# Kernel tuning notes

Measured on AMD Instinct MI355X. Metric: run time of the kernel, lower is better.

## Reference

```python
import jax, jax.numpy as jnp
import numpy as np

B, S, D, H, K = 64, 512, 1024, 1024, 4
DT = 0.05
TAU_MIN, TAU_MAX = 0.01, 10.0


def setup_inputs() -> dict:
    key = jax.random.key(0)
    ks = jax.random.split(key, 5)
    x = jax.random.normal(ks[0], (B, S, D), dtype=jnp.float32)
    # complexity signal [B,1]; positive like a variance
    complexity = jax.random.uniform(ks[1], (B, 1), dtype=jnp.float32) + 0.5
    # orthogonal-ish recurrent weight (scaled normal) and xavier-ish input weight
    W_rec = jax.random.normal(ks[2], (H, H), dtype=jnp.float32) / np.float32(np.sqrt(H))
    W_in = jax.random.normal(ks[3], (D, H), dtype=jnp.float32) * np.float32(np.sqrt(2.0 / (D + H)))
    bias = jnp.zeros((H,), dtype=jnp.float32)
    tau_bands = jnp.logspace(np.log10(TAU_MIN), np.log10(TAU_MAX), K, dtype=jnp.float32)
    mixer_w = jax.random.normal(ks[4], (K, 1), dtype=jnp.float32)  # nn.Linear(1, K).weight
    mixer_b = jnp.zeros((K,), dtype=jnp.float32)                   # nn.Linear(1, K).bias
    return dict(x=x, complexity=complexity, W_rec=W_rec, W_in=W_in,
                bias=bias, tau_bands=tau_bands, mixer_w=mixer_w, mixer_b=mixer_b)


def reference(x, complexity, W_rec, W_in, bias, tau_bands, mixer_w, mixer_b):
    # tau mixing: Linear(1,K) on complexity -> softmax -> convex mix of tau bands
    tau_logits = complexity @ mixer_w.T + mixer_b          # [B, K]
    w = jax.nn.softmax(tau_logits, axis=-1)                # [B, K]
    mixed_tau = jnp.sum(tau_bands[None, :] * w, axis=1)    # [B]
    alpha = jnp.exp(-DT / mixed_tau)[:, None]              # [B, 1] -> broadcasts over H

    h0 = jnp.zeros((x.shape[0], W_rec.shape[0]), dtype=x.dtype)

    def step(h, xt):
        # h_{t+1} = a*h + (1-a)*tanh(h @ W_rec^T + x_t @ W_in^T + b)
        pre = h @ W_rec.T + xt @ W_in.T + bias
        h_new = alpha * h + (1.0 - alpha) * jnp.tanh(pre)
        return h_new, h_new

    h_final, outs = jax.lax.scan(step, h0, jnp.swapaxes(x, 0, 1))  # scan over time
    output = jnp.swapaxes(outs, 0, 1)                               # [B, S, H]
    return output, h_final
```

## Files before the change

kernel.cpp:

```cpp
#include <hip/hip_runtime.h>
#include <math.h>

#define BATCH 64
#define SEQ 512
#define DIM 1024
#define HID 1024
#define KBANDS 4
#define DT_C 0.05f
#define CNT_STRIDE 32

typedef short bf16x8 __attribute__((ext_vector_type(8)));
typedef float f32x4 __attribute__((ext_vector_type(4)));

__device__ __forceinline__ unsigned bf16rn(float x) {
    unsigned u = __float_as_uint(x);
    return (u + 0x7fffu + ((u >> 16) & 1u)) >> 16;
}

__device__ __forceinline__ void splitf(float f, unsigned short* hi, unsigned short* lo) {
    unsigned h = bf16rn(f);
    float r = f - __uint_as_float(h << 16);
    *hi = (unsigned short)h;
    *lo = (unsigned short)bf16rn(r);
}

__device__ __forceinline__ void split_bf16(float4 f, ushort4* hi, ushort4* lo) {
    unsigned short h0, h1, h2, h3, l0, l1, l2, l3;
    splitf(f.x, &h0, &l0); splitf(f.y, &h1, &l1);
    splitf(f.z, &h2, &l2); splitf(f.w, &h3, &l3);
    *hi = make_ushort4(h0, h1, h2, h3);
    *lo = make_ushort4(l0, l1, l2, l3);
}

__global__ void alpha_kernel(const float* __restrict__ complexity,
                             const float* __restrict__ tau_bands,
                             const float* __restrict__ mixer_w,
                             const float* __restrict__ mixer_b,
                             float* __restrict__ alpha) {
    int b = threadIdx.x;
    if (b < BATCH) {
        float c = complexity[b];
        float lg[KBANDS];
        float mx = -1e30f;
        #pragma unroll
        for (int k = 0; k < KBANDS; k++) {
            lg[k] = c * mixer_w[k] + mixer_b[k];
            mx = fmaxf(mx, lg[k]);
        }
        float se = 0.f, tau = 0.f;
        #pragma unroll
        for (int k = 0; k < KBANDS; k++) {
            float e = expf(lg[k] - mx);
            se += e;
            tau += tau_bands[k] * e;
        }
        tau /= se;
        alpha[b] = expf(-DT_C / tau);
    }
}

__global__ __launch_bounds__(256) void win_split(const float* __restrict__ win,
                                                 unsigned short* __restrict__ whi,
                                                 unsigned short* __restrict__ wlo) {
    size_t i = ((size_t)blockIdx.x * 256 + threadIdx.x) * 4;
    float4 f = *(const float4*)(win + i);
    ushort4 h4, l4;
    split_bf16(f, &h4, &l4);
    *(ushort4*)(whi + i) = h4;
    *(ushort4*)(wlo + i) = l4;
}

#define RP 272
#define IG_LDS (4 * 64 * RP)

__global__ __launch_bounds__(256) void in_gemm_mfma(const float* __restrict__ x,
                                                    const unsigned short* __restrict__ whi,
                                                    const unsigned short* __restrict__ wlo,
                                                    const float* __restrict__ bias,
                                                    float* __restrict__ out) {
    extern __shared__ char lg[];
    char* Ahi = lg;
    char* Alo = lg + 64 * RP;
    char* Bhi = lg + 2 * 64 * RP;
    char* Blo = lg + 3 * 64 * RP;

    int tid  = threadIdx.x;
    int m0   = blockIdx.x * 64;
    int n0   = blockIdx.y * 64;
    int lane = tid & 63;
    int w    = tid >> 6;
    int row  = lane & 15;
    int kq   = lane >> 4;

    int srow = tid >> 2;
    int skeg = (tid & 3) * 32;

    const float* xsrc = x + (size_t)(m0 + srow) * 1024 + skeg;
    const unsigned short* bhsrc = whi + (size_t)(n0 + srow) * 1024 + skeg;
    const unsigned short* blsrc = wlo + (size_t)(n0 + srow) * 1024 + skeg;
    char* dah = Ahi + srow * RP + skeg * 2;
    char* dal = Alo + srow * RP + skeg * 2;
    char* dbh = Bhi + srow * RP + skeg * 2;
    char* dbl = Blo + srow * RP + skeg * 2;

    f32x4 acc[4];
    #pragma unroll
    for (int mt = 0; mt < 4; mt++) acc[mt] = (f32x4){0.f, 0.f, 0.f, 0.f};

    for (int k0 = 0; k0 < 1024; k0 += 128) {
        #pragma unroll
        for (int i = 0; i < 8; i++) {
            float4 f = *(const float4*)(xsrc + k0 + i * 4);
            ushort4 h4, l4;
            split_bf16(f, &h4, &l4);
            *(ushort4*)(dah + i * 8) = h4;
            *(ushort4*)(dal + i * 8) = l4;
        }
        #pragma unroll
        for (int i = 0; i < 4; i++) {
            *(float4*)(dbh + i * 16) = *(const float4*)(bhsrc + k0 + i * 8);
            *(float4*)(dbl + i * 16) = *(const float4*)(blsrc + k0 + i * 8);
        }
        __syncthreads();
        #pragma unroll
        for (int ks = 0; ks < 4; ks++) {
            int koff = (ks * 32 + kq * 8) * 2;
            bf16x8 bh = *(const bf16x8*)(Bhi + (w * 16 + row) * RP + koff);
            bf16x8 bl = *(const bf16x8*)(Blo + (w * 16 + row) * RP + koff);
            #pragma unroll
            for (int mt = 0; mt < 4; mt++) {
                bf16x8 ah = *(const bf16x8*)(Ahi + (mt * 16 + row) * RP + koff);
                bf16x8 al = *(const bf16x8*)(Alo + (mt * 16 + row) * RP + koff);
                acc[mt] = __builtin_amdgcn_mfma_f32_16x16x32_bf16(ah, bh, acc[mt], 0, 0, 0);
                acc[mt] = __builtin_amdgcn_mfma_f32_16x16x32_bf16(al, bh, acc[mt], 0, 0, 0);
                acc[mt] = __builtin_amdgcn_mfma_f32_16x16x32_bf16(ah, bl, acc[mt], 0, 0, 0);
            }
        }
        __syncthreads();
    }
    int n = n0 + w * 16 + (lane & 15);
    float bn = bias[n];
    #pragma unroll
    for (int mt = 0; mt < 4; mt++)
        #pragma unroll
        for (int r = 0; r < 4; r++)
            out[(size_t)(m0 + mt * 16 + kq * 4 + r) * 1024 + n] = acc[mt][r] + bn;
}


#define HPITCH 2064
#define LDS_HI  0
#define LDS_LO  33024
#define LDS_RED 66048
#define LDS_TOTAL 70144
#define HB_PLANE 131072
#define HB_SLOT  262144

__global__ __launch_bounds__(256, 1) void recur_coop(const float* __restrict__ Wrec,
                                                     const float* __restrict__ alpha,
                                                     float* __restrict__ out,
                                                     int* __restrict__ cnt,
                                                     unsigned short* __restrict__ hbuf) {
    extern __shared__ char lbase[];

    int tid  = threadIdx.x;
    int bs   = blockIdx.x & 3;
    int js   = blockIdx.x >> 2;
    int lane = tid & 63;
    int w    = tid >> 6;
    int row  = lane & 15;
    int kq   = lane >> 4;

    bf16x8 wh[8], wl[8];
    {
        const float* wsrc = Wrec + (size_t)(js * 16 + row) * HID + w * 256 + kq * 8;
        #pragma unroll
        for (int ks = 0; ks < 8; ks++) {
            float4 f0 = *(const float4*)(wsrc + ks * 32);
            float4 f1 = *(const float4*)(wsrc + ks * 32 + 4);
            union { unsigned short u[8]; bf16x8 v; } H, L;
            splitf(f0.x, &H.u[0], &L.u[0]);
            splitf(f0.y, &H.u[1], &L.u[1]);
            splitf(f0.z, &H.u[2], &L.u[2]);
            splitf(f0.w, &H.u[3], &L.u[3]);
            splitf(f1.x, &H.u[4], &L.u[4]);
            splitf(f1.y, &H.u[5], &L.u[5]);
            splitf(f1.z, &H.u[6], &L.u[6]);
            splitf(f1.w, &H.u[7], &L.u[7]);
            wh[ks] = H.v;
            wl[ks] = L.v;
        }
    }

    int eb = tid >> 4;
    int ej = tid & 15;
    int bglob = bs * 16 + eb;
    int jglob = js * 16 + ej;
    float a_reg = alpha[bglob];
    float om = 1.f - a_reg;
    float* xwp = out + (size_t)bglob * SEQ * HID + jglob;

    int srow = tid >> 4, sl16 = tid & 15;
    const char* hb_lane = (const char*)hbuf + (size_t)(bs * 16 + srow) * 2048 + sl16 * 16;
    char* ph_base = (char*)hbuf + (size_t)bglob * 2048 + jglob * 2;

    float hp = 0.f;
    float* redp = (float*)(lbase + LDS_RED);
    const char* ah_base = lbase + LDS_HI + row * HPITCH + (w * 256 + kq * 8) * 2;
    const char* al_base = lbase + LDS_LO + row * HPITCH + (w * 256 + kq * 8) * 2;
    char* dh = lbase + LDS_HI + srow * HPITCH + sl16 * 16;
    char* dl = lbase + LDS_LO + srow * HPITCH + sl16 * 16;

    for (int t = 0; t < SEQ; t++) {
        float xw = *xwp;
        float sum = 0.f;
        if (t > 0) {
            if (tid == 0) {
                int* cp = cnt + (size_t)((t - 1) * 4 + bs) * CNT_STRIDE;
                int spins = 0;
                while (__hip_atomic_load(cp, __ATOMIC_RELAXED,
                                         __HIP_MEMORY_SCOPE_AGENT) < 64) {
                    __builtin_amdgcn_s_sleep(1);
                    if (++spins >= 8192) {
                        spins = 0;
                        if (__hip_atomic_fetch_add(cp, 0, __ATOMIC_RELAXED,
                                __HIP_MEMORY_SCOPE_AGENT) >= 64) break;
                    }
                }
            }
            __syncthreads();
            {
                const char* bh = hb_lane + (size_t)((t - 1) & 1) * HB_SLOT;
                const char* bl = bh + HB_PLANE;
                float4 v[16];
                #pragma unroll
                for (int it = 0; it < 8; it++)
                    asm volatile("global_load_dwordx4 %0, %1, off offset:%2 sc0 sc1"
                                 : "=v"(v[it]) : "v"(bh), "i"(it * 256) : "memory");
                #pragma unroll
                for (int it = 0; it < 8; it++)
                    asm volatile("global_load_dwordx4 %0, %1, off offset:%2 sc0 sc1"
                                 : "=v"(v[8 + it]) : "v"(bl), "i"(it * 256) : "memory");
                asm volatile("s_waitcnt vmcnt(0)" ::: "memory");
                #pragma unroll
                for (int it = 0; it < 8; it++)
                    *(float4*)(dh + it * 256) = v[it];
                #pragma unroll
                for (int it = 0; it < 8; it++)
                    *(float4*)(dl + it * 256) = v[8 + it];
            }
            __syncthreads();
            f32x4 acc0 = {0.f, 0.f, 0.f, 0.f};
            f32x4 acc1 = {0.f, 0.f, 0.f, 0.f};
            #pragma unroll
            for (int ks = 0; ks < 8; ks++) {
                bf16x8 ah = *(const bf16x8*)(ah_base + ks * 64);
                bf16x8 al = *(const bf16x8*)(al_base + ks * 64);
                if (ks & 1) {
                    acc1 = __builtin_amdgcn_mfma_f32_16x16x32_bf16(ah, wh[ks], acc1, 0, 0, 0);
                    acc1 = __builtin_amdgcn_mfma_f32_16x16x32_bf16(al, wh[ks], acc1, 0, 0, 0);
                    acc1 = __builtin_amdgcn_mfma_f32_16x16x32_bf16(ah, wl[ks], acc1, 0, 0, 0);
                } else {
                    acc0 = __builtin_amdgcn_mfma_f32_16x16x32_bf16(ah, wh[ks], acc0, 0, 0, 0);
                    acc0 = __builtin_amdgcn_mfma_f32_16x16x32_bf16(al, wh[ks], acc0, 0, 0, 0);
                    acc0 = __builtin_amdgcn_mfma_f32_16x16x32_bf16(ah, wl[ks], acc0, 0, 0, 0);
                }
            }
            #pragma unroll
            for (int r = 0; r < 4; r++)
                redp[w * 256 + (kq * 4 + r) * 16 + row] = acc0[r] + acc1[r];
            __syncthreads();
            sum = redp[tid] + redp[256 + tid] + redp[512 + tid] + redp[768 + tid];
        }
        float pre = sum + xw;
        float hn = a_reg * hp + om * tanhf(pre);
        *xwp = hn;
        if (t == SEQ - 1)
            out[(size_t)BATCH * SEQ * HID + (size_t)bglob * HID + jglob] = hn;
        {
            unsigned short hi16, lo16;
            splitf(hn, &hi16, &lo16);
            unsigned hv = hi16, lv = lo16;
            char* ph = ph_base + (size_t)(t & 1) * HB_SLOT;
            char* pl = ph + HB_PLANE;
            asm volatile("global_store_short %0, %1, off sc0 sc1"
                         :: "v"(ph), "v"(hv) : "memory");
            asm volatile("global_store_short %0, %1, off sc0 sc1"
                         :: "v"(pl), "v"(lv) : "memory");
        }
        asm volatile("s_waitcnt vmcnt(0)" ::: "memory");
        __syncthreads();
        if (tid == 0)
            __hip_atomic_fetch_add(cnt + (size_t)(t * 4 + bs) * CNT_STRIDE, 1,
                    __ATOMIC_RELAXED, __HIP_MEMORY_SCOPE_AGENT);
        hp = hn;
        xwp += HID;
    }
}

extern "C" void kernel_launch(void* const* d_in, const int* in_sizes, int n_in,
                              void* d_out, int out_size, void* d_ws, size_t ws_size,
                              hipStream_t stream) {
    const float* x          = (const float*)d_in[0];
    const float* complexity = (const float*)d_in[1];
    const float* Wrec       = (const float*)d_in[2];
    const float* Win        = (const float*)d_in[3];
    const float* bias       = (const float*)d_in[4];
    const float* tau_bands  = (const float*)d_in[5];
    const float* mixer_w    = (const float*)d_in[6];
    const float* mixer_b    = (const float*)d_in[7];
    float* out = (float*)d_out;

    float* alpha = (float*)d_ws;
    int*   cnt   = (int*)((char*)d_ws + 256);
    unsigned short* whi  = (unsigned short*)((char*)d_ws + 266240);
    unsigned short* wlo  = (unsigned short*)((char*)d_ws + 266240 + 2097152);
    unsigned short* hbuf = (unsigned short*)((char*)d_ws + 266240 + 4194304);

    hipMemsetAsync(cnt, 0, SEQ * 4 * CNT_STRIDE * sizeof(int), stream);
    alpha_kernel<<<1, 64, 0, stream>>>(complexity, tau_bands, mixer_w, mixer_b, alpha);
    win_split<<<1024, 256, 0, stream>>>(Win, whi, wlo);

    hipFuncSetAttribute((const void*)in_gemm_mfma,
                        hipFuncAttributeMaxDynamicSharedMemorySize, IG_LDS);
    in_gemm_mfma<<<dim3(512, 16), 256, IG_LDS, stream>>>(x, whi, wlo, bias, out);

    hipFuncSetAttribute((const void*)recur_coop,
                        hipFuncAttributeMaxDynamicSharedMemorySize, LDS_TOTAL);
    void* args[] = { (void*)&Wrec, (void*)&alpha, (void*)&out, (void*)&cnt, (void*)&hbuf };
    hipLaunchCooperativeKernel((void*)recur_coop, dim3(256), dim3(256),
                               args, LDS_TOTAL, stream);
}
```

Measured before the change: 2.544 ms.

## Retile input GEMM so each block covers full N, reading W_in from global

The input-projection GEMM now uses 512-thread blocks that each compute a 64x1024 output slab. A block splits its x tile to bf16 hi/lo pairs once and shares it in LDS across 8 waves. B fragments (W_in hi/lo) are loaded directly from global memory per wave instead of being staged in LDS. This removes the 16x redundant reading and splitting of x across the old N-grid. It risks high register pressure from 32 accumulators per lane and uncoalesced, LDS-free B loads served only by cache.

Result: faster. 2.460 ms (-3.3%).

```diff
diff --git a/kernel.cpp b/kernel.cpp
--- a/kernel.cpp
+++ b/kernel.cpp
@@ -71,9 +71,9 @@
 }
 
 #define RP 272
-#define IG_LDS (4 * 64 * RP)
-
-__global__ __launch_bounds__(256) void in_gemm_mfma(const float* __restrict__ x,
+#define IG_LDS (2 * 64 * RP)
+
+__global__ __launch_bounds__(512) void in_gemm_mfma(const float* __restrict__ x,
                                                     const unsigned short* __restrict__ whi,
                                                     const unsigned short* __restrict__ wlo,
                                                     const float* __restrict__ bias,
@@ -81,70 +81,72 @@
     extern __shared__ char lg[];
     char* Ahi = lg;
     char* Alo = lg + 64 * RP;
-    char* Bhi = lg + 2 * 64 * RP;
-    char* Blo = lg + 3 * 64 * RP;
 
     int tid  = threadIdx.x;
     int m0   = blockIdx.x * 64;
-    int n0   = blockIdx.y * 64;
     int lane = tid & 63;
     int w    = tid >> 6;
     int row  = lane & 15;
     int kq   = lane >> 4;
 
-    int srow = tid >> 2;
-    int skeg = (tid & 3) * 32;
-
+    int srow = tid >> 3;
+    int skeg = (tid & 7) * 16;
     const float* xsrc = x + (size_t)(m0 + srow) * 1024 + skeg;
-    const unsigned short* bhsrc = whi + (size_t)(n0 + srow) * 1024 + skeg;
-    const unsigned short* blsrc = wlo + (size_t)(n0 + srow) * 1024 + skeg;
     char* dah = Ahi + srow * RP + skeg * 2;
     char* dal = Alo + srow * RP + skeg * 2;
-    char* dbh = Bhi + srow * RP + skeg * 2;
-    char* dbl = Blo + srow * RP + skeg * 2;
-
-    f32x4 acc[4];
+
+    f32x4 acc[4][8];
     #pragma unroll
-    for (int mt = 0; mt < 4; mt++) acc[mt] = (f32x4){0.f, 0.f, 0.f, 0.f};
+    for (int mt = 0; mt < 4; mt++)
+        #pragma unroll
+        for (int nt = 0; nt < 8; nt++)
+            acc[mt][nt] = (f32x4){0.f, 0.f, 0.f, 0.f};
 
     for (int k0 = 0; k0 < 1024; k0 += 128) {
         #pragma unroll
-        for (int i = 0; i < 8; i++) {
+        for (int i = 0; i < 4; i++) {
             float4 f = *(const float4*)(xsrc + k0 + i * 4);
             ushort4 h4, l4;
             split_bf16(f, &h4, &l4);
             *(ushort4*)(dah + i * 8) = h4;
             *(ushort4*)(dal + i * 8) = l4;
         }
-        #pragma unroll
-        for (int i = 0; i < 4; i++) {
-            *(float4*)(dbh + i * 16) = *(const float4*)(bhsrc + k0 + i * 8);
-            *(float4*)(dbl + i * 16) = *(const float4*)(blsrc + k0 + i * 8);
-        }
         __syncthreads();
         #pragma unroll
         for (int ks = 0; ks < 4; ks++) {
             int koff = (ks * 32 + kq * 8) * 2;
-            bf16x8 bh = *(const bf16x8*)(Bhi + (w * 16 + row) * RP + koff);
-            bf16x8 bl = *(const bf16x8*)(Blo + (w * 16 + row) * RP + koff);
+            bf16x8 ah[4], al[4];
             #pragma unroll
             for (int mt = 0; mt < 4; mt++) {
-                bf16x8 ah = *(const bf16x8*)(Ahi + (mt * 16 + row) * RP + koff);
-                bf16x8 al = *(const bf16x8*)(Alo + (mt * 16 + row) * RP + koff);
-                acc[mt] = __builtin_amdgcn_mfma_f32_16x16x32_bf16(ah, bh, acc[mt], 0, 0, 0);
-                acc[mt] = __builtin_amdgcn_mfma_f32_16x16x32_bf16(al, bh, acc[mt], 0, 0, 0);
-                acc[mt] = __builtin_amdgcn_mfma_f32_16x16x32_bf16(ah, bl, acc[mt], 0, 0, 0);
+                ah[mt] = *(const bf16x8*)(Ahi + (mt * 16 + row) * RP + koff);
+                al[mt] = *(const bf16x8*)(Alo + (mt * 16 + row) * RP + koff);
+            }
+            #pragma unroll
+            for (int nt = 0; nt < 8; nt++) {
+                size_t boff = (size_t)(w * 128 + nt * 16 + row) * 1024
+                            + k0 + ks * 32 + kq * 8;
+                bf16x8 bh = *(const bf16x8*)(whi + boff);
+                bf16x8 bl = *(const bf16x8*)(wlo + boff);
+                #pragma unroll
+                for (int mt = 0; mt < 4; mt++) {
+                    acc[mt][nt] = __builtin_amdgcn_mfma_f32_16x16x32_bf16(ah[mt], bh, acc[mt][nt], 0, 0, 0);
+                    acc[mt][nt] = __builtin_amdgcn_mfma_f32_16x16x32_bf16(al[mt], bh, acc[mt][nt], 0, 0, 0);
+                    acc[mt][nt] = __builtin_amdgcn_mfma_f32_16x16x32_bf16(ah[mt], bl, acc[mt][nt], 0, 0, 0);
+                }
             }
         }
         __syncthreads();
     }
-    int n = n0 + w * 16 + (lane & 15);
-    float bn = bias[n];
     #pragma unroll
-    for (int mt = 0; mt < 4; mt++)
-        #pragma unroll
-        for (int r = 0; r < 4; r++)
-            out[(size_t)(m0 + mt * 16 + kq * 4 + r) * 1024 + n] = acc[mt][r] + bn;
+    for (int nt = 0; nt < 8; nt++) {
+        int n = w * 128 + nt * 16 + row;
+        float bn = bias[n];
+        #pragma unroll
+        for (int mt = 0; mt < 4; mt++)
+            #pragma unroll
+            for (int r = 0; r < 4; r++)
+                out[(size_t)(m0 + mt * 16 + kq * 4 + r) * 1024 + n] = acc[mt][nt][r] + bn;
+    }
 }
 
 
@@ -323,7 +325,7 @@
 
     hipFuncSetAttribute((const void*)in_gemm_mfma,
                         hipFuncAttributeMaxDynamicSharedMemorySize, IG_LDS);
-    in_gemm_mfma<<<dim3(512, 16), 256, IG_LDS, stream>>>(x, whi, wlo, bias, out);
+    in_gemm_mfma<<<dim3(512), 512, IG_LDS, stream>>>(x, whi, wlo, bias, out);
 
     hipFuncSetAttribute((const void*)recur_coop,
                         hipFuncAttributeMaxDynamicSharedMemorySize, LDS_TOTAL);
```
